# Performance work log

Hardware: AMD Instinct MI355X
Metric: run time of the kernel (lower is better)

Reference implementation:

```python
import jax, jax.numpy as jnp
import numpy as np

D_MODEL, HID, N_NODES, NODE_DIM = 128, 256, 17, 32

def _gelu(x):
    return jax.nn.gelu(x, approximate=False)  # torch nn.GELU default (erf)

def setup_inputs() -> dict:
    key = jax.random.key(0)
    ks = jax.random.split(key, 12)
    B, W = 16, 4096
    x = jax.random.normal(ks[0], (B, W, D_MODEL), dtype=jnp.float32)
    # node_proj: Linear(128,256) -> GELU -> Linear(256, 17*32)
    W1 = jax.random.normal(ks[1], (D_MODEL, HID), dtype=jnp.float32) / np.sqrt(D_MODEL)
    b1 = jnp.zeros((HID,), jnp.float32)
    W2 = jax.random.normal(ks[2], (HID, N_NODES * NODE_DIM), dtype=jnp.float32) / np.sqrt(HID)
    b2 = jnp.zeros((N_NODES * NODE_DIM,), jnp.float32)
    # GAT1
    adj1 = jnp.eye(N_NODES, dtype=jnp.float32) * 5.0 + jax.random.normal(ks[3], (N_NODES, N_NODES), jnp.float32) * 0.05
    Wg1 = jax.random.normal(ks[4], (NODE_DIM, NODE_DIM), dtype=jnp.float32) / np.sqrt(NODE_DIM)
    bg1 = jnp.zeros((NODE_DIM,), jnp.float32)
    # GAT2
    adj2 = jnp.eye(N_NODES, dtype=jnp.float32) * 5.0 + jax.random.normal(ks[5], (N_NODES, N_NODES), jnp.float32) * 0.05
    Wg2 = jax.random.normal(ks[6], (NODE_DIM, NODE_DIM), dtype=jnp.float32) / np.sqrt(NODE_DIM)
    bg2 = jnp.zeros((NODE_DIM,), jnp.float32)
    # coord_proj: Linear(32, 2)
    Wc = jax.random.normal(ks[7], (NODE_DIM, 2), dtype=jnp.float32) / np.sqrt(NODE_DIM)
    bc = jnp.zeros((2,), jnp.float32)
    return {"x": x, "W1": W1, "b1": b1, "W2": W2, "b2": b2,
            "adj1": adj1, "Wg1": Wg1, "bg1": bg1,
            "adj2": adj2, "Wg2": Wg2, "bg2": bg2,
            "Wc": Wc, "bc": bc}

def _gat(nodes, adj_logits, Wg, bg):
    # nodes: [B, W, N, F]
    adj = jax.nn.softmax(adj_logits, axis=-1)          # [N, N]
    mixed = jnp.einsum('ij,bwjf->bwif', adj, nodes)    # graph conv over 17 joints
    return _gelu(mixed @ Wg + bg) + nodes              # linear-GELU + residual

def reference(x, W1, b1, W2, b2, adj1, Wg1, bg1, adj2, Wg2, bg2, Wc, bc):
    B, W, _ = x.shape
    h = _gelu(x @ W1 + b1)                 # [B, W, 256] (dropout inactive at eval)
    nodes = (h @ W2 + b2).reshape(B, W, N_NODES, NODE_DIM)
    out = _gat(nodes, adj1, Wg1, bg1)
    out = _gat(out, adj2, Wg2, bg2)
    return out @ Wc + bc                   # [B, W, 17, 2]
```

## Files before the change

kernel.cpp:

```cpp
#include <hip/hip_runtime.h>
#include <hip/hip_bf16.h>

using bf16 = __hip_bfloat16;
typedef __bf16 bf16x4v __attribute__((ext_vector_type(4)));
typedef __bf16 bf16x8 __attribute__((ext_vector_type(8)));
typedef float f32x4 __attribute__((ext_vector_type(4)));

#define MT 32
#define SX 136
#define SH 264
#define SJ 20
#define TFS 640
#define NTF_ELEMS 20480
#define MS_BASE 20496
#define SMS 36
#define MSW 612
#define S_ELEMS 25936

__device__ __forceinline__ float bf2f(bf16 v) { return __bfloat162float(v); }

__device__ __forceinline__ float gelu_f(float x) {
    float u  = x * fmaf(0.035677408f * x, x, 0.7978845608f);
    float au = fabsf(u);
    float e  = __expf(-2.0f * au);
    float t  = (1.0f - e) * __builtin_amdgcn_rcpf(1.0f + e);
    t = (u < 0.0f) ? -t : t;
    float hx = 0.5f * x;
    return fmaf(hx, t, hx);
}

__device__ __forceinline__ bf16x8 ld8(const bf16* p) {
    return *reinterpret_cast<const bf16x8*>(p);
}
__device__ __forceinline__ bf16x8 ld8u(const bf16* p) {
    bf16x4v lo = *reinterpret_cast<const bf16x4v*>(p);
    bf16x4v hi = *reinterpret_cast<const bf16x4v*>(p + 4);
    return __builtin_shufflevector(lo, hi, 0, 1, 2, 3, 4, 5, 6, 7);
}
__device__ __forceinline__ f32x4 mfma16(bf16x8 a, bf16x8 b, f32x4 c) {
    return __builtin_amdgcn_mfma_f32_16x16x32_bf16(a, b, c, 0, 0, 0);
}

__global__ void prep_kernel(const float* __restrict__ W1, const float* __restrict__ W2,
                            const float* __restrict__ Wg1, const float* __restrict__ Wg2,
                            const float* __restrict__ adj1, const float* __restrict__ adj2,
                            bf16* __restrict__ w1t, bf16* __restrict__ w2t,
                            bf16* __restrict__ wg1t, bf16* __restrict__ wg2t,
                            float* __restrict__ A1f, float* __restrict__ A2f) {
    int idx = blockIdx.x * 256 + threadIdx.x;
    if (idx < 32768) {
        int r = idx >> 8, c = idx & 255;
        w1t[c * 128 + r] = __float2bfloat16(W1[idx]);
    } else if (idx < 172032) {
        int j = idx - 32768;
        int r = j / 544, c = j % 544;
        w2t[c * 256 + r] = __float2bfloat16(W2[j]);
    } else if (idx < 173056) {
        int j = idx - 172032;
        wg1t[(j & 31) * 32 + (j >> 5)] = __float2bfloat16(Wg1[j]);
    } else if (idx < 174080) {
        int j = idx - 173056;
        wg2t[(j & 31) * 32 + (j >> 5)] = __float2bfloat16(Wg2[j]);
    }
    if (blockIdx.x == 0) {
        int t = threadIdx.x;
        if (t < 17 || (t >= 32 && t < 49)) {
            const float* adj = (t < 17) ? adj1 : adj2;
            float*       A   = (t < 17) ? A1f  : A2f;
            int row = (t < 17) ? t : (t - 32);
            float v[17]; float mx = -1e30f;
            for (int j = 0; j < 17; ++j) { v[j] = adj[row * 17 + j]; mx = fmaxf(mx, v[j]); }
            float s = 0.0f;
            for (int j = 0; j < 17; ++j) { v[j] = __expf(v[j] - mx); s += v[j]; }
            float inv = 1.0f / s;
            for (int j = 0; j < 17; ++j) A[row * 17 + j] = v[j] * inv;
        }
    }
}

__global__ __launch_bounds__(512, 4)
void gat_main(const float* __restrict__ x,
              const float* __restrict__ b1, const float* __restrict__ b2,
              const float* __restrict__ bg1, const float* __restrict__ bg2,
              const bf16* __restrict__ w1t, const bf16* __restrict__ w2t,
              const bf16* __restrict__ wg1t, const bf16* __restrict__ wg2t,
              const float* __restrict__ A1, const float* __restrict__ A2,
              const float* __restrict__ Wc, const float* __restrict__ bc,
              float* __restrict__ out) {
    __shared__ alignas(16) bf16 S[S_ELEMS];
    bf16* xs = S;
    bf16* hs = S + 4352;

    const int tid  = threadIdx.x;
    const int w    = tid >> 6;
    const int lane = tid & 63;
    const int l    = lane & 15;
    const int q    = lane >> 4;
    const int t0   = blockIdx.x * MT;

    for (int c = tid; c < 1024; c += 512) {
        int row = c >> 5, c4 = c & 31;
        const float4 v = *reinterpret_cast<const float4*>(x + (size_t)(t0 + row) * 128 + c4 * 4);
        bf16 tmp[4] = { __float2bfloat16(v.x), __float2bfloat16(v.y),
                        __float2bfloat16(v.z), __float2bfloat16(v.w) };
        *reinterpret_cast<ushort4*>(xs + row * SX + c4 * 4) =
            *reinterpret_cast<const ushort4*>(tmp);
    }
    __syncthreads();

    for (int nt = w * 2; nt < w * 2 + 2; ++nt) {
        int n = nt * 16 + l;
        bf16x8 bfr[4];
        const bf16* wp = w1t + n * 128 + q * 8;
#pragma unroll
        for (int kf = 0; kf < 4; ++kf) bfr[kf] = ld8(wp + kf * 32);
        float bias = b1[n];
#pragma unroll
        for (int mt = 0; mt < 2; ++mt) {
            f32x4 acc = {0.f, 0.f, 0.f, 0.f};
            const bf16* ap = xs + (mt * 16 + l) * SX + q * 8;
#pragma unroll
            for (int kf = 0; kf < 4; ++kf)
                acc = mfma16(ld8(ap + kf * 32), bfr[kf], acc);
            int trow = mt * 16 + q * 4;
#pragma unroll
            for (int r = 0; r < 4; ++r)
                hs[(trow + r) * SH + n] = __float2bfloat16(gelu_f(acc[r] + bias));
        }
    }
    __syncthreads();

    {
        bf16x8 af[2][8];
#pragma unroll
        for (int mt = 0; mt < 2; ++mt)
#pragma unroll
            for (int kf = 0; kf < 8; ++kf)
                af[mt][kf] = ld8(hs + (mt * 16 + l) * SH + kf * 32 + q * 8);
        __syncthreads();

        for (int z = tid; z < 3072; z += 512) {
            int row = z / 3, k = z - row * 3;
            S[row * SJ + 17 + k] = __float2bfloat16(0.f);
        }
        if (tid < 16) S[NTF_ELEMS + tid] = __float2bfloat16(0.f);

        for (int nt = w; nt < 34; nt += 8) {
            int n = nt * 16 + l;
            float bias = b2[n];
            int i = n >> 5, f = n & 31;
            f32x4 a0 = {0.f, 0.f, 0.f, 0.f}, a1 = {0.f, 0.f, 0.f, 0.f};
            const bf16* wp = w2t + n * 256 + q * 8;
#pragma unroll
            for (int kf = 0; kf < 8; ++kf) {
                bf16x8 bfr = ld8(wp + kf * 32);
                a0 = mfma16(af[0][kf], bfr, a0);
                a1 = mfma16(af[1][kf], bfr, a1);
            }
#pragma unroll
            for (int mt = 0; mt < 2; ++mt) {
                const f32x4 acc = mt ? a1 : a0;
#pragma unroll
                for (int r = 0; r < 4; ++r) {
                    int t = mt * 16 + q * 4 + r;
                    S[t * TFS + f * SJ + i] = __float2bfloat16(acc[r] + bias);
                }
            }
        }
    }
    __syncthreads();

    bf16* ms_w = S + MS_BASE + w * MSW;

    for (int g = 0; g < 2; ++g) {
        const float* A  = g ? A2 : A1;
        const bf16* wgt = g ? wg2t : wg1t;
        const float* bg = g ? bg2 : bg1;

        bf16x8 mixB[2];
#pragma unroll
        for (int nt = 0; nt < 2; ++nt) {
            int i = nt * 16 + l;
            bf16 tmp[8];
#pragma unroll
            for (int e = 0; e < 8; ++e) {
                int j = q * 8 + e;
                float v = (i < 17 && j < 17) ? A[i * 17 + j] : 0.0f;
                tmp[e] = __float2bfloat16(v);
            }
            mixB[nt] = *reinterpret_cast<bf16x8*>(tmp);
        }
        bf16x8 wfr[2];
#pragma unroll
        for (int nt = 0; nt < 2; ++nt) wfr[nt] = ld8(wgt + (nt * 16 + l) * 32 + q * 8);
        float bgf[2] = { bg[l], bg[16 + l] };

        for (int c = 0; c < 4; ++c) {
            const int T = w * 4 + c;

#pragma unroll
            for (int mt2 = 0; mt2 < 2; ++mt2) {
                int R = T * 32 + mt2 * 16 + l;
                bf16x8 afr = ld8u(S + R * SJ + q * 8);
                int f0 = mt2 * 16 + q * 4;
#pragma unroll
                for (int nt = 0; nt < 2; ++nt) {
                    f32x4 acc = {0.f, 0.f, 0.f, 0.f};
                    acc = mfma16(afr, mixB[nt], acc);
                    int i = nt * 16 + l;
                    if (i < 17) {
                        union { ushort4 u; bf16 b[4]; } pk;
#pragma unroll
                        for (int r = 0; r < 4; ++r) pk.b[r] = __float2bfloat16(acc[r]);
                        *reinterpret_cast<ushort4*>(ms_w + i * SMS + f0) = pk.u;
                    }
                }
            }

#pragma unroll
            for (int mt = 0; mt < 2; ++mt) {
                bf16x8 afr = ld8u(ms_w + (mt * 16 + l) * SMS + q * 8);
                int i0 = mt * 16 + q * 4;
#pragma unroll
                for (int nt = 0; nt < 2; ++nt) {
                    f32x4 acc = {0.f, 0.f, 0.f, 0.f};
                    acc = mfma16(afr, wfr[nt], acc);
                    int fp = nt * 16 + l;
                    if (i0 < 17) {
                        bf16* p = S + T * TFS + fp * SJ + i0;
                        union { ushort4 u; bf16 b[4]; } old, nw;
                        old.u = *reinterpret_cast<const ushort4*>(p);
#pragma unroll
                        for (int r = 0; r < 4; ++r) {
                            float v = gelu_f(acc[r] + bgf[nt]) + bf2f(old.b[r]);
                            if (i0 + r > 16) v = 0.0f;
                            nw.b[r] = __float2bfloat16(v);
                        }
                        *reinterpret_cast<ushort4*>(p) = nw.u;
                    }
                }
            }
        }
    }

    for (int s = lane; s < 68; s += 64) {
        int tl = s / 17, i = s - tl * 17;
        int t  = w * 4 + tl;
        const bf16* gp = S + t * TFS + i;
        float o0 = bc[0], o1 = bc[1];
#pragma unroll
        for (int f = 0; f < 32; ++f) {
            float v = bf2f(gp[f * SJ]);
            o0 = fmaf(v, Wc[f * 2 + 0], o0);
            o1 = fmaf(v, Wc[f * 2 + 1], o1);
        }
        float2 pr = { o0, o1 };
        reinterpret_cast<float2*>(out)[(size_t)(t0 + t) * 17 + i] = pr;
    }
}

extern "C" void kernel_launch(void* const* d_in, const int* in_sizes, int n_in,
                              void* d_out, int out_size, void* d_ws, size_t ws_size,
                              hipStream_t stream) {
    const float* x    = (const float*)d_in[0];
    const float* W1   = (const float*)d_in[1];
    const float* b1   = (const float*)d_in[2];
    const float* W2   = (const float*)d_in[3];
    const float* b2   = (const float*)d_in[4];
    const float* adj1 = (const float*)d_in[5];
    const float* Wg1  = (const float*)d_in[6];
    const float* bg1  = (const float*)d_in[7];
    const float* adj2 = (const float*)d_in[8];
    const float* Wg2  = (const float*)d_in[9];
    const float* bg2  = (const float*)d_in[10];
    const float* Wc   = (const float*)d_in[11];
    const float* bc   = (const float*)d_in[12];

    char* ws = (char*)d_ws;
    bf16*  w1t  = (bf16*)(ws + 0);
    bf16*  w2t  = (bf16*)(ws + 65536);
    bf16*  wg1t = (bf16*)(ws + 344064);
    bf16*  wg2t = (bf16*)(ws + 346112);
    float* A1f  = (float*)(ws + 348160);
    float* A2f  = (float*)(ws + 349376);

    prep_kernel<<<680, 256, 0, stream>>>(W1, W2, Wg1, Wg2, adj1, adj2,
                                         w1t, w2t, wg1t, wg2t, A1f, A2f);

    const int tokens = 16 * 4096;
    gat_main<<<tokens / MT, 512, 0, stream>>>(x, b1, b2, bg1, bg2,
                                              w1t, w2t, wg1t, wg2t,
                                              A1f, A2f, Wc, bc, (float*)d_out);
}
```

Baseline: 236.0 us.

## Pack two tokens per GAT tile, precompute mix fragments, simplify GELU

```diff
diff --git a/kernel.cpp b/kernel.cpp
--- a/kernel.cpp
+++ b/kernel.cpp
@@ -14,17 +14,14 @@
 #define NTF_ELEMS 20480
 #define MS_BASE 20496
 #define SMS 36
-#define MSW 612
-#define S_ELEMS 25936
+#define MSW 1224
+#define S_ELEMS 30800
 
 __device__ __forceinline__ float bf2f(bf16 v) { return __bfloat162float(v); }
 
 __device__ __forceinline__ float gelu_f(float x) {
-    float u  = x * fmaf(0.035677408f * x, x, 0.7978845608f);
-    float au = fabsf(u);
-    float e  = __expf(-2.0f * au);
-    float t  = (1.0f - e) * __builtin_amdgcn_rcpf(1.0f + e);
-    t = (u < 0.0f) ? -t : t;
+    float z  = x * fmaf(0.10294343f * x, x, 2.3022082f);
+    float t  = fmaf(-2.0f, __builtin_amdgcn_rcpf(exp2f(z) + 1.0f), 1.0f);
     float hx = 0.5f * x;
     return fmaf(hx, t, hx);
 }
@@ -78,13 +75,27 @@
     }
 }
 
+__global__ void prep_mixb(const float* __restrict__ A1f, const float* __restrict__ A2f,
+                          bf16* __restrict__ mb) {
+    int idx = blockIdx.x * 256 + threadIdx.x;
+    if (idx < 2048) {
+        int g = idx >> 10, rem = idx & 1023;
+        int nt = rem >> 9, lane = (rem >> 3) & 63, e = rem & 7;
+        int i = nt * 16 + (lane & 15);
+        int j = (lane >> 4) * 8 + e;
+        const float* A = g ? A2f : A1f;
+        float v = (i < 17 && j < 17) ? A[i * 17 + j] : 0.0f;
+        mb[idx] = __float2bfloat16(v);
+    }
+}
+
 __global__ __launch_bounds__(512, 4)
 void gat_main(const float* __restrict__ x,
               const float* __restrict__ b1, const float* __restrict__ b2,
               const float* __restrict__ bg1, const float* __restrict__ bg2,
               const bf16* __restrict__ w1t, const bf16* __restrict__ w2t,
               const bf16* __restrict__ wg1t, const bf16* __restrict__ wg2t,
-              const float* __restrict__ A1, const float* __restrict__ A2,
+              const bf16* __restrict__ mb,
               const float* __restrict__ Wc, const float* __restrict__ bc,
               float* __restrict__ out) {
     __shared__ alignas(16) bf16 S[S_ELEMS];
@@ -170,73 +181,69 @@
     }
     __syncthreads();
 
-    bf16* ms_w = S + MS_BASE + w * MSW;
+    bf16* ms_p = S + MS_BASE + w * MSW;
 
     for (int g = 0; g < 2; ++g) {
-        const float* A  = g ? A2 : A1;
+        const bf16* mbg = mb + g * 1024;
         const bf16* wgt = g ? wg2t : wg1t;
         const float* bg = g ? bg2 : bg1;
 
-        bf16x8 mixB[2];
-#pragma unroll
-        for (int nt = 0; nt < 2; ++nt) {
-            int i = nt * 16 + l;
-            bf16 tmp[8];
-#pragma unroll
-            for (int e = 0; e < 8; ++e) {
-                int j = q * 8 + e;
-                float v = (i < 17 && j < 17) ? A[i * 17 + j] : 0.0f;
-                tmp[e] = __float2bfloat16(v);
-            }
-            mixB[nt] = *reinterpret_cast<bf16x8*>(tmp);
-        }
+        bf16x8 mixB[2] = { ld8(mbg + lane * 8), ld8(mbg + 512 + lane * 8) };
         bf16x8 wfr[2];
 #pragma unroll
         for (int nt = 0; nt < 2; ++nt) wfr[nt] = ld8(wgt + (nt * 16 + l) * 32 + q * 8);
         float bgf[2] = { bg[l], bg[16 + l] };
 
-        for (int c = 0; c < 4; ++c) {
-            const int T = w * 4 + c;
-
-#pragma unroll
-            for (int mt2 = 0; mt2 < 2; ++mt2) {
-                int R = T * 32 + mt2 * 16 + l;
+        for (int p = 0; p < 2; ++p) {
+            const int T0 = w * 4 + p * 2;
+
+#pragma unroll
+            for (int u = 0; u < 4; ++u) {
+                int tl = u >> 1, ft = u & 1;
+                int R = (T0 + tl) * 32 + ft * 16 + l;
                 bf16x8 afr = ld8u(S + R * SJ + q * 8);
-                int f0 = mt2 * 16 + q * 4;
+                int f0 = ft * 16 + q * 4;
 #pragma unroll
                 for (int nt = 0; nt < 2; ++nt) {
                     f32x4 acc = {0.f, 0.f, 0.f, 0.f};
                     acc = mfma16(afr, mixB[nt], acc);
-                    int i = nt * 16 + l;
-                    if (i < 17) {
-                        union { ushort4 u; bf16 b[4]; } pk;
-#pragma unroll
-                        for (int r = 0; r < 4; ++r) pk.b[r] = __float2bfloat16(acc[r]);
-                        *reinterpret_cast<ushort4*>(ms_w + i * SMS + f0) = pk.u;
+                    union { ushort4 u4; bf16 b[4]; } pk;
+#pragma unroll
+                    for (int r = 0; r < 4; ++r) pk.b[r] = __float2bfloat16(acc[r]);
+                    if (nt == 0) {
+                        *reinterpret_cast<ushort4*>(ms_p + (tl * 16 + l) * SMS + f0) = pk.u4;
+                    } else if (l == 0) {
+                        *reinterpret_cast<ushort4*>(ms_p + (32 + tl) * SMS + f0) = pk.u4;
                     }
                 }
             }
 
 #pragma unroll
-            for (int mt = 0; mt < 2; ++mt) {
-                bf16x8 afr = ld8u(ms_w + (mt * 16 + l) * SMS + q * 8);
-                int i0 = mt * 16 + q * 4;
+            for (int mt = 0; mt < 3; ++mt) {
+                bf16x8 afr = ld8u(ms_p + (mt * 16 + l) * SMS + q * 8);
 #pragma unroll
                 for (int nt = 0; nt < 2; ++nt) {
                     f32x4 acc = {0.f, 0.f, 0.f, 0.f};
                     acc = mfma16(afr, wfr[nt], acc);
                     int fp = nt * 16 + l;
-                    if (i0 < 17) {
-                        bf16* p = S + T * TFS + fp * SJ + i0;
-                        union { ushort4 u; bf16 b[4]; } old, nw;
-                        old.u = *reinterpret_cast<const ushort4*>(p);
+                    if (mt < 2) {
+                        int i0 = q * 4;
+                        bf16* ptr = S + (T0 + mt) * TFS + fp * SJ + i0;
+                        union { ushort4 u4; bf16 b[4]; } old, nw;
+                        old.u4 = *reinterpret_cast<const ushort4*>(ptr);
 #pragma unroll
                         for (int r = 0; r < 4; ++r) {
                             float v = gelu_f(acc[r] + bgf[nt]) + bf2f(old.b[r]);
-                            if (i0 + r > 16) v = 0.0f;
                             nw.b[r] = __float2bfloat16(v);
                         }
-                        *reinterpret_cast<ushort4*>(p) = nw.u;
+                        *reinterpret_cast<ushort4*>(ptr) = nw.u4;
+                    } else if (q == 0) {
+#pragma unroll
+                        for (int r = 0; r < 2; ++r) {
+                            bf16* pp = S + (T0 + r) * TFS + fp * SJ + 16;
+                            float v = gelu_f(acc[r] + bgf[nt]) + bf2f(*pp);
+                            *pp = __float2bfloat16(v);
+                        }
                     }
                 }
             }
@@ -283,12 +290,14 @@
     bf16*  wg2t = (bf16*)(ws + 346112);
     float* A1f  = (float*)(ws + 348160);
     float* A2f  = (float*)(ws + 349376);
+    bf16*  mbt  = (bf16*)(ws + 350592);
 
     prep_kernel<<<680, 256, 0, stream>>>(W1, W2, Wg1, Wg2, adj1, adj2,
                                          w1t, w2t, wg1t, wg2t, A1f, A2f);
+    prep_mixb<<<8, 256, 0, stream>>>(A1f, A2f, mbt);
 
     const int tokens = 16 * 4096;
     gat_main<<<tokens / MT, 512, 0, stream>>>(x, b1, b2, bg1, bg2,
-                                              w1t, w2t, wg1t, wg2t,
-                                              A1f, A2f, Wc, bc, (float*)d_out);
-}
+                                              w1t, w2t, wg1t, wg2t, mbt,
+                                              Wc, bc, (float*)d_out);
+}
```

New measurement: 218.1 us. 1.08x faster.
